# Performance work log

Hardware: AMD Instinct MI355X
Metric: run time of the kernel (lower is better)

## Reference

```python
import jax, jax.numpy as jnp
import numpy as np

E = 8          # moe_expert_count
CAPACITY = 1024  # per-expert capacity C = S / E (capacity factor 1)


def _top1_gate(features, wg):
    """Top-1 gate with capacity, returning combine_weights [S,E,C],
    dispatch_mask [S,E,C], and load-balancing aux loss (standard Switch/BASE-style gate
    matching the (l_aux, combine_weights, dispatch_mask) interface used by BaseLayer)."""
    S, M = features.shape
    logits = features @ wg                      # [S, E]
    gates = jax.nn.softmax(logits, axis=-1)     # [S, E]
    idx = jnp.argmax(gates, axis=-1)            # [S] expert assignment
    mask1 = jax.nn.one_hot(idx, E, dtype=features.dtype)  # [S, E]
    # position of each token inside its expert's buffer (0-based, order of arrival)
    locations = jnp.cumsum(mask1, axis=0) - mask1          # [S, E]
    loc = jnp.sum(locations * mask1, axis=1).astype(jnp.int32)  # [S]
    keep = (loc < CAPACITY).astype(features.dtype)          # drop overflow tokens
    mask1 = mask1 * keep[:, None]
    gate_s = jnp.sum(gates * mask1, axis=1)                 # [S] gate prob of kept tokens
    loc_oh = jax.nn.one_hot(loc, CAPACITY, dtype=features.dtype)  # [S, C]
    combine = gate_s[:, None, None] * mask1[:, :, None] * loc_oh[:, None, :]  # [S,E,C]
    dispatch = (combine > 0).astype(features.dtype)
    # load-balance aux loss: E * sum(mean_prob_e * frac_tokens_e)
    me = jnp.mean(gates, axis=0)
    ce = jnp.mean(mask1, axis=0)
    l_aux = jnp.sum(me * ce) * E
    return l_aux, combine, dispatch


def setup_inputs() -> dict:
    key = jax.random.key(0)
    k0, k1, k2, k3 = jax.random.split(key, 4)
    B, T, M, H = 4, 2048, 512, 1024
    return {
        "hidden_states": jax.random.normal(k0, (B, T, M), dtype=jnp.float32),
        "wg": jax.random.normal(k1, (M, E), dtype=jnp.float32) * 0.02,
        "w1": jax.random.normal(k2, (E, M, H), dtype=jnp.float32) * 0.02,
        "b1": jnp.zeros((E, H), dtype=jnp.float32),
        "w2": jax.random.normal(k3, (E, H, M), dtype=jnp.float32) * 0.02,
        "b2": jnp.zeros((E, M), dtype=jnp.float32),
    }


def reference(hidden_states, wg, w1, b1, w2, b2):
    B, T, M = hidden_states.shape
    feats = hidden_states.reshape(-1, M)            # [S, M]
    l_aux, combine, dispatch = _top1_gate(feats, wg)
    # dense one-hot dispatch matmul: (E*C, S) @ (S, M) -> [E, C, M]
    dispatched = jnp.einsum('sec,sm->ecm', dispatch, feats)
    # per-expert FFN (BaseSublayer: Linear -> ReLU -> Linear)
    h = jax.nn.relu(jnp.einsum('ecm,emh->ech', dispatched, w1) + b1[:, None, :])
    expert_out = jnp.einsum('ech,ehn->ecn', h, w2) + b2[:, None, :]  # [E, C, M]
    # dense combine matmul: (S, E*C) @ (E*C, M) -> [S, M]
    combined = jnp.einsum('sec,ecn->sn', combine, expert_out)
    return combined.reshape(B, T, -1), l_aux
```

## Files before the change

kernel.cpp:

```cpp
#include <hip/hip_runtime.h>

#define S_TOK 8192
#define M_DIM 512
#define E_NUM 8
#define CAP   1024
#define H_DIM 1024
#define NGATE_BLK (S_TOK / 4)

typedef __attribute__((ext_vector_type(8))) short bf16x8;
typedef __attribute__((ext_vector_type(16))) float f32x16;

__device__ static inline unsigned short f2bf(float f) {
    unsigned int u = __float_as_uint(f);
    unsigned int r = (u + 0x7fffu + ((u >> 16) & 1u)) >> 16;
    return (unsigned short)r;
}

__device__ static inline void async_copy16(const void* g, void* l) {
    __builtin_amdgcn_global_load_lds(
        (const __attribute__((address_space(1))) void*)g,
        (__attribute__((address_space(3))) void*)l, 16, 0, 0);
}

__global__ __launch_bounds__(256) void prep_kernel(
    const float* __restrict__ feats, const float* __restrict__ wg,
    int* __restrict__ idx, float* __restrict__ gate_top,
    float* __restrict__ gates_psum, unsigned short* __restrict__ xb,
    const float* __restrict__ w1, unsigned short* __restrict__ w1t,
    const float* __restrict__ w2, unsigned short* __restrict__ w2t)
{
    __shared__ float gsh[4][8];
    __shared__ float tile[64][65];

    if (blockIdx.x < NGATE_BLK) {
        const int wave = threadIdx.x >> 6;
        const int lane = threadIdx.x & 63;
        const int s = blockIdx.x * 4 + wave;

        const float* xrow = feats + (size_t)s * M_DIM;
        const int m0 = lane * 8;

        const float4 va = *(const float4*)(xrow + m0);
        const float4 vb = *(const float4*)(xrow + m0 + 4);
        float xv[8] = {va.x, va.y, va.z, va.w, vb.x, vb.y, vb.z, vb.w};

        {
            bf16x8 o;
#pragma unroll
            for (int j = 0; j < 8; ++j) o[j] = (short)f2bf(xv[j]);
            *(bf16x8*)(xb + (size_t)s * M_DIM + m0) = o;
            if (blockIdx.x == 0 && wave == 0) {
                bf16x8 z = (bf16x8){0,0,0,0,0,0,0,0};
                *(bf16x8*)(xb + (size_t)S_TOK * M_DIM + m0) = z;
            }
        }

        float p[8];
#pragma unroll
        for (int e = 0; e < 8; ++e) p[e] = 0.f;
#pragma unroll
        for (int j = 0; j < 8; ++j) {
            const float4 wa = *(const float4*)(wg + (m0 + j) * 8);
            const float4 wb2 = *(const float4*)(wg + (m0 + j) * 8 + 4);
            const float x = xv[j];
            p[0] += x * wa.x;  p[1] += x * wa.y;  p[2] += x * wa.z;  p[3] += x * wa.w;
            p[4] += x * wb2.x; p[5] += x * wb2.y; p[6] += x * wb2.z; p[7] += x * wb2.w;
        }
#pragma unroll
        for (int e = 0; e < 8; ++e) {
            float v = p[e];
#pragma unroll
            for (int off = 1; off < 64; off <<= 1) v += __shfl_xor(v, off, 64);
            p[e] = v;
        }
        if (lane == 0) {
            float mx = p[0];
#pragma unroll
            for (int e = 1; e < 8; ++e) mx = fmaxf(mx, p[e]);
            float ex[8], sum = 0.f;
#pragma unroll
            for (int e = 0; e < 8; ++e) { ex[e] = expf(p[e] - mx); sum += ex[e]; }
            const float inv = 1.0f / sum;
            int best = 0; float bl = p[0];
#pragma unroll
            for (int e = 1; e < 8; ++e) { if (p[e] > bl) { bl = p[e]; best = e; } }
#pragma unroll
            for (int e = 0; e < 8; ++e) gsh[wave][e] = ex[e] * inv;
            idx[s] = best;
            gate_top[s] = ex[best] * inv;
        }
        __syncthreads();
        if (threadIdx.x < 8) {
            const int e = threadIdx.x;
            gates_psum[blockIdx.x * 8 + e] =
                gsh[0][e] + gsh[1][e] + gsh[2][e] + gsh[3][e];
        }
    } else {
        int b = blockIdx.x - NGATE_BLK;
        const float* src; unsigned short* dst;
        int e, k0, n0, K, N;
        if (b < 1024) {
            e = b >> 7; const int rem = b & 127;
            k0 = (rem >> 4) * 64; n0 = (rem & 15) * 64;
            K = 512; N = 1024; src = w1; dst = w1t;
        } else {
            b -= 1024;
            e = b >> 7; const int rem = b & 127;
            k0 = (rem >> 3) * 64; n0 = (rem & 7) * 64;
            K = 1024; N = 512; src = w2; dst = w2t;
        }
        const int t = threadIdx.x;
        const int r = t >> 4, c4 = (t & 15) * 4;
#pragma unroll
        for (int i = 0; i < 4; ++i) {
            const int row = r + i * 16;
            const float4 v = *(const float4*)(src + ((size_t)e * K + k0 + row) * N + n0 + c4);
            tile[row][c4 + 0] = v.x; tile[row][c4 + 1] = v.y;
            tile[row][c4 + 2] = v.z; tile[row][c4 + 3] = v.w;
        }
        __syncthreads();
#pragma unroll
        for (int i = 0; i < 4; ++i) {
            const int row = r + i * 16;
            ushort4 o;
            o.x = f2bf(tile[c4 + 0][row]); o.y = f2bf(tile[c4 + 1][row]);
            o.z = f2bf(tile[c4 + 2][row]); o.w = f2bf(tile[c4 + 3][row]);
            *(ushort4*)(dst + ((size_t)e * N + n0 + row) * K + k0 + c4) = o;
        }
    }
}

__global__ __launch_bounds__(256) void scan_kernel(
    const int* __restrict__ idx, const float* __restrict__ gate_top,
    const float* __restrict__ gates_psum,
    float* __restrict__ gate_final, int* __restrict__ token_list,
    int* __restrict__ kept, float* __restrict__ out)
{
    __shared__ int   cnts[256][9];
    __shared__ float wpart[4][8];
    __shared__ int   totals[8];
    __shared__ int   sdrop[7168];
    __shared__ int   dropctr;

    const int t = threadIdx.x;
    const int wv = t >> 6, ln = t & 63;
    const int base = t * 32;

    for (int i = t; i < E_NUM * CAP; i += 256) token_list[i] = S_TOK;
    if (t == 0) dropctr = 0;

    int c[8];
#pragma unroll
    for (int e = 0; e < 8; ++e) c[e] = 0;
    for (int i = 0; i < 32; ++i) {
        const int ei = idx[base + i];
#pragma unroll
        for (int e = 0; e < 8; ++e) c[e] += (ei == e) ? 1 : 0;
    }
    float g[8];
#pragma unroll
    for (int e = 0; e < 8; ++e) g[e] = 0.f;
    for (int i = 0; i < NGATE_BLK / 256; ++i) {
        const float* gp = gates_psum + (size_t)(t + 256 * i) * 8;
        const float4 a = *(const float4*)gp;
        const float4 b = *(const float4*)(gp + 4);
        g[0] += a.x; g[1] += a.y; g[2] += a.z; g[3] += a.w;
        g[4] += b.x; g[5] += b.y; g[6] += b.z; g[7] += b.w;
    }
#pragma unroll
    for (int e = 0; e < 8; ++e) cnts[t][e] = c[e];
#pragma unroll
    for (int e = 0; e < 8; ++e) {
        float v = g[e];
#pragma unroll
        for (int off = 1; off < 64; off <<= 1) v += __shfl_xor(v, off, 64);
        if (ln == 0) wpart[wv][e] = v;
    }
    __syncthreads();

#pragma unroll
    for (int ee = 0; ee < 2; ++ee) {
        const int e = wv * 2 + ee;
        int off = 0;
#pragma unroll
        for (int seg = 0; seg < 4; ++seg) {
            const int r = seg * 64 + ln;
            const int v = cnts[r][e];
            int incl = v;
#pragma unroll
            for (int d = 1; d < 64; d <<= 1) {
                const int nn = __shfl_up(incl, d, 64);
                if (ln >= d) incl += nn;
            }
            cnts[r][e] = incl - v + off;
            off += __shfl(incl, 63, 64);
        }
        if (ln == 0) {
            totals[e] = off;
            kept[e] = off < CAP ? off : CAP;
        }
    }
    __syncthreads();

    if (t == 0) {
        float l = 0.f;
        for (int e = 0; e < 8; ++e) {
            const float ms = wpart[0][e] + wpart[1][e] + wpart[2][e] + wpart[3][e];
            const int ke = totals[e] < CAP ? totals[e] : CAP;
            l += (ms / (float)S_TOK) * ((float)ke / (float)S_TOK);
        }
        out[(size_t)S_TOK * M_DIM] = l * (float)E_NUM;
    }

    int rc[8];
#pragma unroll
    for (int e = 0; e < 8; ++e) rc[e] = cnts[t][e];

    for (int i = 0; i < 32; ++i) {
        const int s = base + i;
        const int ei = idx[s];
        int loc = 0;
#pragma unroll
        for (int e = 0; e < 8; ++e) {
            if (ei == e) { loc = rc[e]; rc[e] = rc[e] + 1; }
        }
        const bool keepit = loc < CAP;
        gate_final[s] = keepit ? gate_top[s] : 0.f;
        if (keepit) {
            token_list[ei * CAP + loc] = s;
        } else {
            const int d = atomicAdd(&dropctr, 1);
            sdrop[d] = s;
        }
    }
    __syncthreads();

    const int nd = dropctr;
    for (int d = wv; d < nd; d += 4) {
        const int s = sdrop[d];
        float4 z = make_float4(0.f, 0.f, 0.f, 0.f);
        *(float4*)(out + (size_t)s * M_DIM + ln * 4) = z;
        *(float4*)(out + (size_t)s * M_DIM + 256 + ln * 4) = z;
    }
}

__global__ __launch_bounds__(256, 4) void ffn1_mfma(
    const unsigned short* __restrict__ xb, const unsigned short* __restrict__ w1t,
    const float* __restrict__ b1, const int* __restrict__ tok,
    const int* __restrict__ kept, unsigned short* __restrict__ h)
{
    const int b = blockIdx.x;
    const int e = b & 7;
    const int r = b >> 3;
    const int ct = r >> 4, nt = r & 15;
    const int c0 = ct * 128, n0 = nt * 64;
    if (c0 >= kept[e]) return;

    __shared__ __align__(16) short Alds[128 * 64];
    __shared__ __align__(16) short Blds[64 * 64];
    __shared__ int srow[128];

    const int t = threadIdx.x;
    const int wave = t >> 6, lane = t & 63;
    const int wm = wave & 1, wn = wave >> 1;
    const int l31 = lane & 31, kh = lane >> 5;

    if (t < 128) srow[t] = tok[e * CAP + c0 + t];
    __syncthreads();

    f32x16 acc[2];
#pragma unroll
    for (int mg = 0; mg < 2; ++mg)
#pragma unroll
        for (int i = 0; i < 16; ++i) acc[mg][i] = 0.f;

    for (int kb = 0; kb < M_DIM; kb += 64) {
        __syncthreads();
#pragma unroll
        for (int i = 0; i < 4; ++i) {
            const int lin = (i * 4 + wave) * 64 + lane;
            const int row = lin >> 3;
            const int ch = (lin & 7) ^ (row & 7);
            async_copy16(xb + (size_t)srow[row] * M_DIM + kb + ch * 8,
                         &Alds[lin * 8]);
        }
#pragma unroll
        for (int i = 0; i < 2; ++i) {
            const int lin = (i * 4 + wave) * 64 + lane;
            const int row = lin >> 3;
            const int ch = (lin & 7) ^ (row & 7);
            async_copy16(w1t + ((size_t)e * H_DIM + n0 + row) * M_DIM + kb + ch * 8,
                         &Blds[lin * 8]);
        }
        __syncthreads();

#pragma unroll
        for (int kk = 0; kk < 64; kk += 16) {
            const int ch = (kk >> 3) + kh;
            bf16x8 af[2], bfv;
#pragma unroll
            for (int mg = 0; mg < 2; ++mg) {
                const int R = wm * 64 + mg * 32 + l31;
                af[mg] = *(const bf16x8*)(&Alds[(R * 8 + (ch ^ (R & 7))) * 8]);
            }
            {
                const int R = wn * 32 + l31;
                bfv = *(const bf16x8*)(&Blds[(R * 8 + (ch ^ (R & 7))) * 8]);
            }
#pragma unroll
            for (int mg = 0; mg < 2; ++mg)
                acc[mg] = __builtin_amdgcn_mfma_f32_32x32x16_bf16(
                    af[mg], bfv, acc[mg], 0, 0, 0);
        }
    }

    const int col = n0 + wn * 32 + l31;
    const float bias = b1[e * H_DIM + col];
#pragma unroll
    for (int mg = 0; mg < 2; ++mg) {
#pragma unroll
        for (int reg = 0; reg < 16; ++reg) {
            const int rowl = wm * 64 + mg * 32 + (reg & 3) + 8 * (reg >> 2) + 4 * kh;
            const float v = fmaxf(acc[mg][reg] + bias, 0.f);
            h[(size_t)(e * CAP + c0 + rowl) * H_DIM + col] = f2bf(v);
        }
    }
}

__global__ __launch_bounds__(256, 4) void ffn2_mfma(
    const unsigned short* __restrict__ h, const unsigned short* __restrict__ w2t,
    const float* __restrict__ b2, const int* __restrict__ tok,
    const int* __restrict__ kept, const float* __restrict__ gate_final,
    float* __restrict__ out)
{
    const int b = blockIdx.x;
    const int e = b & 7;
    const int r = b >> 3;
    const int ct = r >> 3, nt = r & 7;
    const int c0 = ct * 64, n0 = nt * 64;
    if (c0 >= kept[e]) return;

    __shared__ __align__(16) short Alds[64 * 64];
    __shared__ __align__(16) short Blds[64 * 64];
    __shared__ int   stok[64];
    __shared__ float sgf[64];

    const int t = threadIdx.x;
    const int wave = t >> 6, lane = t & 63;
    const int wm = wave & 1, wn = wave >> 1;
    const int l31 = lane & 31, kh = lane >> 5;

    if (t < 64) {
        const int tk = tok[e * CAP + c0 + t];
        stok[t] = tk;
        sgf[t] = (tk != S_TOK) ? gate_final[tk] : 0.f;
    }

    f32x16 acc;
#pragma unroll
    for (int i = 0; i < 16; ++i) acc[i] = 0.f;

    for (int kb = 0; kb < H_DIM; kb += 64) {
        __syncthreads();
#pragma unroll
        for (int i = 0; i < 2; ++i) {
            const int lin = (i * 4 + wave) * 64 + lane;
            const int row = lin >> 3;
            const int ch = (lin & 7) ^ (row & 7);
            async_copy16(h + (size_t)(e * CAP + c0 + row) * H_DIM + kb + ch * 8,
                         &Alds[lin * 8]);
        }
#pragma unroll
        for (int i = 0; i < 2; ++i) {
            const int lin = (i * 4 + wave) * 64 + lane;
            const int row = lin >> 3;
            const int ch = (lin & 7) ^ (row & 7);
            async_copy16(w2t + ((size_t)e * M_DIM + n0 + row) * H_DIM + kb + ch * 8,
                         &Blds[lin * 8]);
        }
        __syncthreads();

#pragma unroll
        for (int kk = 0; kk < 64; kk += 16) {
            const int ch = (kk >> 3) + kh;
            bf16x8 af, bfv;
            {
                const int R = wm * 32 + l31;
                af = *(const bf16x8*)(&Alds[(R * 8 + (ch ^ (R & 7))) * 8]);
            }
            {
                const int R = wn * 32 + l31;
                bfv = *(const bf16x8*)(&Blds[(R * 8 + (ch ^ (R & 7))) * 8]);
            }
            acc = __builtin_amdgcn_mfma_f32_32x32x16_bf16(af, bfv, acc, 0, 0, 0);
        }
    }

    const int col = n0 + wn * 32 + l31;
    const float bias = b2[e * M_DIM + col];
#pragma unroll
    for (int reg = 0; reg < 16; ++reg) {
        const int slot = wm * 32 + (reg & 3) + 8 * (reg >> 2) + 4 * kh;
        const int tokid = stok[slot];
        if (tokid != S_TOK) {
            out[(size_t)tokid * M_DIM + col] = sgf[slot] * (acc[reg] + bias);
        }
    }
}

extern "C" void kernel_launch(void* const* d_in, const int* in_sizes, int n_in,
                              void* d_out, int out_size, void* d_ws, size_t ws_size,
                              hipStream_t stream) {
    const float* feats = (const float*)d_in[0];
    const float* wg    = (const float*)d_in[1];
    const float* w1    = (const float*)d_in[2];
    const float* b1    = (const float*)d_in[3];
    const float* w2    = (const float*)d_in[4];
    const float* b2    = (const float*)d_in[5];
    float* out = (float*)d_out;

    char* ws = (char*)d_ws;
    size_t off = 0;
    unsigned short* h   = (unsigned short*)(ws + off); off += (size_t)E_NUM * CAP * H_DIM * 2;
    unsigned short* xb  = (unsigned short*)(ws + off); off += (size_t)(S_TOK + 1) * M_DIM * 2;
    unsigned short* w1t = (unsigned short*)(ws + off); off += (size_t)E_NUM * H_DIM * M_DIM * 2;
    unsigned short* w2t = (unsigned short*)(ws + off); off += (size_t)E_NUM * M_DIM * H_DIM * 2;
    int*   idx        = (int*)(ws + off);   off += (size_t)S_TOK * 4;
    float* gate_top   = (float*)(ws + off); off += (size_t)S_TOK * 4;
    float* gate_final = (float*)(ws + off); off += (size_t)S_TOK * 4;
    float* gates_psum = (float*)(ws + off); off += (size_t)NGATE_BLK * 8 * 4;
    int*   token_list = (int*)(ws + off);   off += (size_t)S_TOK * 4;
    int*   kept       = (int*)(ws + off);   off += 64;
    (void)ws_size; (void)n_in; (void)in_sizes;

    prep_kernel<<<NGATE_BLK + 2048, 256, 0, stream>>>(
        feats, wg, idx, gate_top, gates_psum, xb, w1, w1t, w2, w2t);
    scan_kernel<<<1, 256, 0, stream>>>(idx, gate_top, gates_psum, gate_final,
                                       token_list, kept, out);
    ffn1_mfma<<<1024, 256, 0, stream>>>(xb, w1t, b1, token_list, kept, h);
    ffn2_mfma<<<1024, 256, 0, stream>>>(h, w2t, b2, token_list, kept,
                                        gate_final, out);
}
```

Before: 177.4 us.

## Overlap single-block scan with weight transpose by merging them into one kernel

Splits the prep kernel into a gate-only kernel and moves the weight transpose/bf16 conversion into the same launch as the serial routing scan. Block 0 runs the scan while the other 2048 blocks convert w1/w2, so the long single-block scan no longer sits alone on the GPU. Shared memory is a union sized to the larger of the two uses, which raises LDS per block for the transpose blocks and may lower their occupancy.

```diff
diff --git a/kernel.cpp b/kernel.cpp
--- a/kernel.cpp
+++ b/kernel.cpp
@@ -22,81 +22,202 @@
         (__attribute__((address_space(3))) void*)l, 16, 0, 0);
 }
 
-__global__ __launch_bounds__(256) void prep_kernel(
+__global__ __launch_bounds__(256) void gate_kernel(
     const float* __restrict__ feats, const float* __restrict__ wg,
     int* __restrict__ idx, float* __restrict__ gate_top,
-    float* __restrict__ gates_psum, unsigned short* __restrict__ xb,
+    float* __restrict__ gates_psum, unsigned short* __restrict__ xb)
+{
+    __shared__ float gsh[4][8];
+    const int wave = threadIdx.x >> 6;
+    const int lane = threadIdx.x & 63;
+    const int s = blockIdx.x * 4 + wave;
+
+    const float* xrow = feats + (size_t)s * M_DIM;
+    const int m0 = lane * 8;
+
+    const float4 va = *(const float4*)(xrow + m0);
+    const float4 vb = *(const float4*)(xrow + m0 + 4);
+    float xv[8] = {va.x, va.y, va.z, va.w, vb.x, vb.y, vb.z, vb.w};
+
+    {
+        bf16x8 o;
+#pragma unroll
+        for (int j = 0; j < 8; ++j) o[j] = (short)f2bf(xv[j]);
+        *(bf16x8*)(xb + (size_t)s * M_DIM + m0) = o;
+        if (blockIdx.x == 0 && wave == 0) {
+            bf16x8 z = (bf16x8){0,0,0,0,0,0,0,0};
+            *(bf16x8*)(xb + (size_t)S_TOK * M_DIM + m0) = z;
+        }
+    }
+
+    float p[8];
+#pragma unroll
+    for (int e = 0; e < 8; ++e) p[e] = 0.f;
+#pragma unroll
+    for (int j = 0; j < 8; ++j) {
+        const float4 wa = *(const float4*)(wg + (m0 + j) * 8);
+        const float4 wb2 = *(const float4*)(wg + (m0 + j) * 8 + 4);
+        const float x = xv[j];
+        p[0] += x * wa.x;  p[1] += x * wa.y;  p[2] += x * wa.z;  p[3] += x * wa.w;
+        p[4] += x * wb2.x; p[5] += x * wb2.y; p[6] += x * wb2.z; p[7] += x * wb2.w;
+    }
+#pragma unroll
+    for (int e = 0; e < 8; ++e) {
+        float v = p[e];
+#pragma unroll
+        for (int off = 1; off < 64; off <<= 1) v += __shfl_xor(v, off, 64);
+        p[e] = v;
+    }
+    if (lane == 0) {
+        float mx = p[0];
+#pragma unroll
+        for (int e = 1; e < 8; ++e) mx = fmaxf(mx, p[e]);
+        float ex[8], sum = 0.f;
+#pragma unroll
+        for (int e = 0; e < 8; ++e) { ex[e] = expf(p[e] - mx); sum += ex[e]; }
+        const float inv = 1.0f / sum;
+        int best = 0; float bl = p[0];
+#pragma unroll
+        for (int e = 1; e < 8; ++e) { if (p[e] > bl) { bl = p[e]; best = e; } }
+#pragma unroll
+        for (int e = 0; e < 8; ++e) gsh[wave][e] = ex[e] * inv;
+        idx[s] = best;
+        gate_top[s] = ex[best] * inv;
+    }
+    __syncthreads();
+    if (threadIdx.x < 8) {
+        const int e = threadIdx.x;
+        gates_psum[blockIdx.x * 8 + e] =
+            gsh[0][e] + gsh[1][e] + gsh[2][e] + gsh[3][e];
+    }
+}
+
+struct ScanSmem {
+    int   cnts[256][9];
+    float wpart[4][8];
+    int   totals[8];
+    int   sdrop[7168];
+    int   dropctr;
+};
+#define CONV_SMEM (64 * 65 * 4)
+#define MID_SMEM ((sizeof(ScanSmem) > CONV_SMEM) ? sizeof(ScanSmem) : CONV_SMEM)
+
+__global__ __launch_bounds__(256) void mid_kernel(
+    const int* __restrict__ idx, const float* __restrict__ gate_top,
+    const float* __restrict__ gates_psum,
+    float* __restrict__ gate_final, int* __restrict__ token_list,
+    int* __restrict__ kept, float* __restrict__ out,
     const float* __restrict__ w1, unsigned short* __restrict__ w1t,
     const float* __restrict__ w2, unsigned short* __restrict__ w2t)
 {
-    __shared__ float gsh[4][8];
-    __shared__ float tile[64][65];
-
-    if (blockIdx.x < NGATE_BLK) {
-        const int wave = threadIdx.x >> 6;
-        const int lane = threadIdx.x & 63;
-        const int s = blockIdx.x * 4 + wave;
-
-        const float* xrow = feats + (size_t)s * M_DIM;
-        const int m0 = lane * 8;
-
-        const float4 va = *(const float4*)(xrow + m0);
-        const float4 vb = *(const float4*)(xrow + m0 + 4);
-        float xv[8] = {va.x, va.y, va.z, va.w, vb.x, vb.y, vb.z, vb.w};
-
-        {
-            bf16x8 o;
-#pragma unroll
-            for (int j = 0; j < 8; ++j) o[j] = (short)f2bf(xv[j]);
-            *(bf16x8*)(xb + (size_t)s * M_DIM + m0) = o;
-            if (blockIdx.x == 0 && wave == 0) {
-                bf16x8 z = (bf16x8){0,0,0,0,0,0,0,0};
-                *(bf16x8*)(xb + (size_t)S_TOK * M_DIM + m0) = z;
-            }
-        }
-
-        float p[8];
-#pragma unroll
-        for (int e = 0; e < 8; ++e) p[e] = 0.f;
-#pragma unroll
-        for (int j = 0; j < 8; ++j) {
-            const float4 wa = *(const float4*)(wg + (m0 + j) * 8);
-            const float4 wb2 = *(const float4*)(wg + (m0 + j) * 8 + 4);
-            const float x = xv[j];
-            p[0] += x * wa.x;  p[1] += x * wa.y;  p[2] += x * wa.z;  p[3] += x * wa.w;
-            p[4] += x * wb2.x; p[5] += x * wb2.y; p[6] += x * wb2.z; p[7] += x * wb2.w;
-        }
+    __shared__ __align__(16) char smem[MID_SMEM];
+
+    if (blockIdx.x == 0) {
+        ScanSmem& S = *reinterpret_cast<ScanSmem*>(smem);
+        const int t = threadIdx.x;
+        const int wv = t >> 6, ln = t & 63;
+        const int base = t * 32;
+
+        for (int i = t; i < E_NUM * CAP; i += 256) token_list[i] = S_TOK;
+        if (t == 0) S.dropctr = 0;
+
+        int c[8];
+#pragma unroll
+        for (int e = 0; e < 8; ++e) c[e] = 0;
+        for (int i = 0; i < 32; ++i) {
+            const int ei = idx[base + i];
+#pragma unroll
+            for (int e = 0; e < 8; ++e) c[e] += (ei == e) ? 1 : 0;
+        }
+        float g[8];
+#pragma unroll
+        for (int e = 0; e < 8; ++e) g[e] = 0.f;
+        for (int i = 0; i < NGATE_BLK / 256; ++i) {
+            const float* gp = gates_psum + (size_t)(t + 256 * i) * 8;
+            const float4 a = *(const float4*)gp;
+            const float4 b = *(const float4*)(gp + 4);
+            g[0] += a.x; g[1] += a.y; g[2] += a.z; g[3] += a.w;
+            g[4] += b.x; g[5] += b.y; g[6] += b.z; g[7] += b.w;
+        }
+#pragma unroll
+        for (int e = 0; e < 8; ++e) S.cnts[t][e] = c[e];
 #pragma unroll
         for (int e = 0; e < 8; ++e) {
-            float v = p[e];
+            float v = g[e];
 #pragma unroll
             for (int off = 1; off < 64; off <<= 1) v += __shfl_xor(v, off, 64);
-            p[e] = v;
-        }
-        if (lane == 0) {
-            float mx = p[0];
-#pragma unroll
-            for (int e = 1; e < 8; ++e) mx = fmaxf(mx, p[e]);
-            float ex[8], sum = 0.f;
-#pragma unroll
-            for (int e = 0; e < 8; ++e) { ex[e] = expf(p[e] - mx); sum += ex[e]; }
-            const float inv = 1.0f / sum;
-            int best = 0; float bl = p[0];
-#pragma unroll
-            for (int e = 1; e < 8; ++e) { if (p[e] > bl) { bl = p[e]; best = e; } }
-#pragma unroll
-            for (int e = 0; e < 8; ++e) gsh[wave][e] = ex[e] * inv;
-            idx[s] = best;
-            gate_top[s] = ex[best] * inv;
-        }
-        __syncthreads();
-        if (threadIdx.x < 8) {
-            const int e = threadIdx.x;
-            gates_psum[blockIdx.x * 8 + e] =
-                gsh[0][e] + gsh[1][e] + gsh[2][e] + gsh[3][e];
+            if (ln == 0) S.wpart[wv][e] = v;
+        }
+        __syncthreads();
+
+#pragma unroll
+        for (int ee = 0; ee < 2; ++ee) {
+            const int e = wv * 2 + ee;
+            int off = 0;
+#pragma unroll
+            for (int seg = 0; seg < 4; ++seg) {
+                const int r = seg * 64 + ln;
+                const int v = S.cnts[r][e];
+                int incl = v;
+#pragma unroll
+                for (int d = 1; d < 64; d <<= 1) {
+                    const int nn = __shfl_up(incl, d, 64);
+                    if (ln >= d) incl += nn;
+                }
+                S.cnts[r][e] = incl - v + off;
+                off += __shfl(incl, 63, 64);
+            }
+            if (ln == 0) {
+                S.totals[e] = off;
+                kept[e] = off < CAP ? off : CAP;
+            }
+        }
+        __syncthreads();
+
+        if (t == 0) {
+            float l = 0.f;
+            for (int e = 0; e < 8; ++e) {
+                const float ms = S.wpart[0][e] + S.wpart[1][e] +
+                                 S.wpart[2][e] + S.wpart[3][e];
+                const int ke = S.totals[e] < CAP ? S.totals[e] : CAP;
+                l += (ms / (float)S_TOK) * ((float)ke / (float)S_TOK);
+            }
+            out[(size_t)S_TOK * M_DIM] = l * (float)E_NUM;
+        }
+
+        int rc[8];
+#pragma unroll
+        for (int e = 0; e < 8; ++e) rc[e] = S.cnts[t][e];
+
+        for (int i = 0; i < 32; ++i) {
+            const int s = base + i;
+            const int ei = idx[s];
+            int loc = 0;
+#pragma unroll
+            for (int e = 0; e < 8; ++e) {
+                if (ei == e) { loc = rc[e]; rc[e] = rc[e] + 1; }
+            }
+            const bool keepit = loc < CAP;
+            gate_final[s] = keepit ? gate_top[s] : 0.f;
+            if (keepit) {
+                token_list[ei * CAP + loc] = s;
+            } else {
+                const int d = atomicAdd(&S.dropctr, 1);
+                S.sdrop[d] = s;
+            }
+        }
+        __syncthreads();
+
+        const int nd = S.dropctr;
+        for (int d = wv; d < nd; d += 4) {
+            const int s = S.sdrop[d];
+            float4 z = make_float4(0.f, 0.f, 0.f, 0.f);
+            *(float4*)(out + (size_t)s * M_DIM + ln * 4) = z;
+            *(float4*)(out + (size_t)s * M_DIM + 256 + ln * 4) = z;
         }
     } else {
-        int b = blockIdx.x - NGATE_BLK;
+        float (*tile)[65] = reinterpret_cast<float(*)[65]>(smem);
+        int b = blockIdx.x - 1;
         const float* src; unsigned short* dst;
         int e, k0, n0, K, N;
         if (b < 1024) {
@@ -127,120 +248,6 @@
             o.z = f2bf(tile[c4 + 2][row]); o.w = f2bf(tile[c4 + 3][row]);
             *(ushort4*)(dst + ((size_t)e * N + n0 + row) * K + k0 + c4) = o;
         }
-    }
-}
-
-__global__ __launch_bounds__(256) void scan_kernel(
-    const int* __restrict__ idx, const float* __restrict__ gate_top,
-    const float* __restrict__ gates_psum,
-    float* __restrict__ gate_final, int* __restrict__ token_list,
-    int* __restrict__ kept, float* __restrict__ out)
-{
-    __shared__ int   cnts[256][9];
-    __shared__ float wpart[4][8];
-    __shared__ int   totals[8];
-    __shared__ int   sdrop[7168];
-    __shared__ int   dropctr;
-
-    const int t = threadIdx.x;
-    const int wv = t >> 6, ln = t & 63;
-    const int base = t * 32;
-
-    for (int i = t; i < E_NUM * CAP; i += 256) token_list[i] = S_TOK;
-    if (t == 0) dropctr = 0;
-
-    int c[8];
-#pragma unroll
-    for (int e = 0; e < 8; ++e) c[e] = 0;
-    for (int i = 0; i < 32; ++i) {
-        const int ei = idx[base + i];
-#pragma unroll
-        for (int e = 0; e < 8; ++e) c[e] += (ei == e) ? 1 : 0;
-    }
-    float g[8];
-#pragma unroll
-    for (int e = 0; e < 8; ++e) g[e] = 0.f;
-    for (int i = 0; i < NGATE_BLK / 256; ++i) {
-        const float* gp = gates_psum + (size_t)(t + 256 * i) * 8;
-        const float4 a = *(const float4*)gp;
-        const float4 b = *(const float4*)(gp + 4);
-        g[0] += a.x; g[1] += a.y; g[2] += a.z; g[3] += a.w;
-        g[4] += b.x; g[5] += b.y; g[6] += b.z; g[7] += b.w;
-    }
-#pragma unroll
-    for (int e = 0; e < 8; ++e) cnts[t][e] = c[e];
-#pragma unroll
-    for (int e = 0; e < 8; ++e) {
-        float v = g[e];
-#pragma unroll
-        for (int off = 1; off < 64; off <<= 1) v += __shfl_xor(v, off, 64);
-        if (ln == 0) wpart[wv][e] = v;
-    }
-    __syncthreads();
-
-#pragma unroll
-    for (int ee = 0; ee < 2; ++ee) {
-        const int e = wv * 2 + ee;
-        int off = 0;
-#pragma unroll
-        for (int seg = 0; seg < 4; ++seg) {
-            const int r = seg * 64 + ln;
-            const int v = cnts[r][e];
-            int incl = v;
-#pragma unroll
-            for (int d = 1; d < 64; d <<= 1) {
-                const int nn = __shfl_up(incl, d, 64);
-                if (ln >= d) incl += nn;
-            }
-            cnts[r][e] = incl - v + off;
-            off += __shfl(incl, 63, 64);
-        }
-        if (ln == 0) {
-            totals[e] = off;
-            kept[e] = off < CAP ? off : CAP;
-        }
-    }
-    __syncthreads();
-
-    if (t == 0) {
-        float l = 0.f;
-        for (int e = 0; e < 8; ++e) {
-            const float ms = wpart[0][e] + wpart[1][e] + wpart[2][e] + wpart[3][e];
-            const int ke = totals[e] < CAP ? totals[e] : CAP;
-            l += (ms / (float)S_TOK) * ((float)ke / (float)S_TOK);
-        }
-        out[(size_t)S_TOK * M_DIM] = l * (float)E_NUM;
-    }
-
-    int rc[8];
-#pragma unroll
-    for (int e = 0; e < 8; ++e) rc[e] = cnts[t][e];
-
-    for (int i = 0; i < 32; ++i) {
-        const int s = base + i;
-        const int ei = idx[s];
-        int loc = 0;
-#pragma unroll
-        for (int e = 0; e < 8; ++e) {
-            if (ei == e) { loc = rc[e]; rc[e] = rc[e] + 1; }
-        }
-        const bool keepit = loc < CAP;
-        gate_final[s] = keepit ? gate_top[s] : 0.f;
-        if (keepit) {
-            token_list[ei * CAP + loc] = s;
-        } else {
-            const int d = atomicAdd(&dropctr, 1);
-            sdrop[d] = s;
-        }
-    }
-    __syncthreads();
-
-    const int nd = dropctr;
-    for (int d = wv; d < nd; d += 4) {
-        const int s = sdrop[d];
-        float4 z = make_float4(0.f, 0.f, 0.f, 0.f);
-        *(float4*)(out + (size_t)s * M_DIM + ln * 4) = z;
-        *(float4*)(out + (size_t)s * M_DIM + 256 + ln * 4) = z;
     }
 }
 
@@ -433,10 +440,11 @@
     int*   kept       = (int*)(ws + off);   off += 64;
     (void)ws_size; (void)n_in; (void)in_sizes;
 
-    prep_kernel<<<NGATE_BLK + 2048, 256, 0, stream>>>(
-        feats, wg, idx, gate_top, gates_psum, xb, w1, w1t, w2, w2t);
-    scan_kernel<<<1, 256, 0, stream>>>(idx, gate_top, gates_psum, gate_final,
-                                       token_list, kept, out);
+    gate_kernel<<<NGATE_BLK, 256, 0, stream>>>(feats, wg, idx, gate_top,
+                                               gates_psum, xb);
+    mid_kernel<<<1 + 2048, 256, 0, stream>>>(idx, gate_top, gates_psum,
+                                             gate_final, token_list, kept, out,
+                                             w1, w1t, w2, w2t);
     ffn1_mfma<<<1024, 256, 0, stream>>>(xb, w1t, b1, token_list, kept, h);
     ffn2_mfma<<<1024, 256, 0, stream>>>(h, w2t, b2, token_list, kept,
                                         gate_final, out);
```

New measurement: 178.4 us. About the same (+0.5%).
